# Optimization experiments

Measured on AMD Instinct MI355X. Metric: run time of the kernel, lower is better.

## Reference

```python
import jax, jax.numpy as jnp
import numpy as np

N0, N1 = 30000, 20000
N = N0 + N1
E = 400000
H0, H1, H2 = 4, 4, 1
DH = 64            # num_hidden
NC = 16            # num_classes
IN = 128           # per-type input feature dim
SLOPE = 0.2        # leaky relu negative slope


def setup_inputs() -> dict:
    key = jax.random.key(0)
    ks = iter(jax.random.split(key, 48))
    rn = lambda shape, s=0.05: jax.random.normal(next(ks), shape, jnp.float32) * s
    ri = lambda shape: jax.random.randint(next(ks), shape, 0, N, jnp.int32)
    inp = {
        'features0': rn((N0, IN), 1.0),
        'features1': rn((N1, IN), 1.0),
        'fc_w0': rn((IN, DH)), 'fc_b0': jnp.zeros((DH,), jnp.float32),
        'fc_w1': rn((IN, DH)), 'fc_b1': jnp.zeros((DH,), jnp.float32),
        'mix_w': jnp.zeros((2, 3, 2), jnp.float32),  # (n_types, num_layers+1, n_graphs)
        # GATConv params stacked over the 2 relation graphs
        'W0': rn((2, DH, H0 * DH)), 'al0': rn((2, H0, DH), 0.1), 'ar0': rn((2, H0, DH), 0.1), 'b0': jnp.zeros((2, H0 * DH), jnp.float32),
        'W1': rn((2, H0 * DH, H1 * DH)), 'al1': rn((2, H1, DH), 0.1), 'ar1': rn((2, H1, DH), 0.1), 'b1': jnp.zeros((2, H1 * DH), jnp.float32),
        'W2': rn((2, H1 * DH, H2 * NC)), 'al2': rn((2, H2, NC), 0.1), 'ar2': rn((2, H2, NC), 0.1), 'b2': jnp.zeros((2, H2 * NC), jnp.float32),
        'res2': rn((2, H1 * DH, H2 * NC)),  # res_fc for last layer (in != out*heads)
        'src0': ri((E,)), 'dst0': ri((E,)),
        'src1': ri((E,)), 'dst1': ri((E,)),
    }
    return inp


def gat_conv(h, src, dst, W, al, ar, b, H, D, res_mode, res_w, act):
    # h: (N, in)  ->  (N, H, D)
    feat = (h @ W).reshape(N, H, D)
    el = jnp.sum(feat * al, axis=-1)   # (N, H)
    er = jnp.sum(feat * ar, axis=-1)   # (N, H)
    e = jax.nn.leaky_relu(el[src] + er[dst], SLOPE)  # (E, H)
    # edge softmax over incoming edges of each dst node
    m = jax.ops.segment_max(e, dst, num_segments=N)
    ex = jnp.exp(e - m[dst])
    den = jax.ops.segment_sum(ex, dst, num_segments=N)
    alpha = ex / den[dst]                              # (E, H)
    out = jax.ops.segment_sum(feat[src] * alpha[..., None], dst, num_segments=N)
    if res_mode == 'id':
        out = out + h.reshape(N, H, D)
    elif res_mode == 'fc':
        out = out + (h @ res_w).reshape(N, H, D)
    out = out + b.reshape(1, H, D)
    return jax.nn.elu(out) if act else out


def _forward(features0, features1, fc_w0, fc_b0, fc_w1, fc_b1, mix_w,
             W0, al0, ar0, b0, W1, al1, ar1, b1, W2, al2, ar2, b2, res2,
             src0, dst0, src1, dst1):
    nt = jnp.concatenate([jnp.zeros(N0, jnp.int32), jnp.ones(N1, jnp.int32)])
    w = jax.nn.softmax(mix_w, axis=2)  # (types, layers+1, graphs)
    h = jnp.concatenate([features0 @ fc_w0 + fc_b0, features1 @ fc_w1 + fc_b1], axis=0)
    srcs, dsts = (src0, src1), (dst0, dst1)
    layers = [
        (W0, al0, ar0, b0, H0, DH, None, True),
        (W1, al1, ar1, b1, H1, DH, 'id', True),
    ]
    for l, (W, al, ar, b, H, D, rm, act) in enumerate(layers):
        acc = 0.
        for i in range(2):
            o = gat_conv(h, srcs[i], dsts[i], W[i], al[i], ar[i], b[i], H, D, rm, None, act)
            acc = acc + o.reshape(N, H * D) * w[nt, l, i][:, None]
        h = acc
    logits = 0.
    for i in range(2):
        o = gat_conv(h, srcs[i], dsts[i], W2[i], al2[i], ar2[i], b2[i], H2, NC, 'fc', res2[i], False)
        logits = logits + o.mean(axis=1) * w[nt, 2, i][:, None]
    return logits


def reference(features0, features1, fc_w0, fc_b0, fc_w1, fc_b1, mix_w,
              W0, al0, ar0, b0, W1, al1, ar1, b1, W2, al2, ar2, b2, res2,
              src0, dst0, src1, dst1):
    return _forward(features0, features1, fc_w0, fc_b0, fc_w1, fc_b1, mix_w,
                    W0, al0, ar0, b0, W1, al1, ar1, b1, W2, al2, ar2, b2, res2,
                    src0, dst0, src1, dst1)
```

## Files before the change

### kernel.cpp

```cpp
#include <hip/hip_runtime.h>
#include <hip/hip_bf16.h>

#define NN   50000
#define NN0  30000
#define EE   400000
#define NB_SCAN ((NN + 1023) / 1024)
#define NB_E  ((EE + 255) / 256)
#define NRT   3125
#define NGRP  ((NRT + 3) / 4)
#define NGRP2 1563
#define NT0   1875

typedef unsigned short u16;
typedef unsigned int   u32;

typedef __attribute__((ext_vector_type(8))) __bf16 bf16x8;
typedef __attribute__((ext_vector_type(4))) float  f32x4;
typedef __attribute__((ext_vector_type(2))) float  f32x2;

__device__ __forceinline__ float bf2f(u16 u){ return __uint_as_float(((u32)u)<<16); }
__device__ __forceinline__ float lo16(u32 u){ return __uint_as_float(u<<16); }
__device__ __forceinline__ float hi16(u32 u){ return __uint_as_float(u & 0xffff0000u); }
__device__ __forceinline__ u16 f2bf(float f){
  u32 x = __float_as_uint(f);
  x += 0x7fffu + ((x>>16)&1u);
  return (u16)(x>>16);
}
__device__ __forceinline__ float elu_f(float x){ return x>0.f ? x : __expf(x)-1.f; }
__device__ __forceinline__ float lrelu(float x){ return x>0.f ? x : 0.2f*x; }
__device__ __forceinline__ bf16x8 ld_frag(const u16* p){
  uint4 v = *(const uint4*)p;
  return __builtin_bit_cast(bf16x8, v);
}
__device__ __forceinline__ bf16x8 cvt8(const float* p){
  float4 u = ((const float4*)p)[0];
  float4 v = ((const float4*)p)[1];
  u32 w0 = (u32)f2bf(u.x) | ((u32)f2bf(u.y)<<16);
  u32 w1 = (u32)f2bf(u.z) | ((u32)f2bf(u.w)<<16);
  u32 w2 = (u32)f2bf(v.x) | ((u32)f2bf(v.y)<<16);
  u32 w3 = (u32)f2bf(v.z) | ((u32)f2bf(v.w)<<16);
  uint4 r{w0,w1,w2,w3};
  return __builtin_bit_cast(bf16x8, r);
}
__device__ __forceinline__ u32   ld_u16o (const char* b, u32 o){ return *(const u16*)(b + o); }
__device__ __forceinline__ u32   ld_u32o (const char* b, u32 o){ return *(const u32*)(b + o); }
__device__ __forceinline__ float ld_f32o (const char* b, u32 o){ return *(const float*)(b + o); }
__device__ __forceinline__ float4 ld_f4o (const char* b, u32 o){ return *(const float4*)(b + o); }
__device__ __forceinline__ uint4  ld_u4o (const char* b, u32 o){ return *(const uint4*)(b + o); }
__device__ __forceinline__ void acc8pk(f32x2* p, float& den, float x, uint4 f){
  den += x;
  f32x2 xx = {x, x};
  f32x2 t0 = {lo16(f.x), hi16(f.x)};
  f32x2 t1 = {lo16(f.y), hi16(f.y)};
  f32x2 t2 = {lo16(f.z), hi16(f.z)};
  f32x2 t3 = {lo16(f.w), hi16(f.w)};
  p[0] = __builtin_elementwise_fma(t0, xx, p[0]);
  p[1] = __builtin_elementwise_fma(t1, xx, p[1]);
  p[2] = __builtin_elementwise_fma(t2, xx, p[2]);
  p[3] = __builtin_elementwise_fma(t3, xx, p[3]);
}
__device__ __forceinline__ void acc2x4(f32x2* a, f32x2& d01, f32x2& d23, float4 x, u32 w){
  f32x2 v = {lo16(w), hi16(w)};
  f32x2 x0 = {x.x, x.x}, x1 = {x.y, x.y}, x2 = {x.z, x.z}, x3 = {x.w, x.w};
  a[0] = __builtin_elementwise_fma(v, x0, a[0]);
  a[1] = __builtin_elementwise_fma(v, x1, a[1]);
  a[2] = __builtin_elementwise_fma(v, x2, a[2]);
  a[3] = __builtin_elementwise_fma(v, x3, a[3]);
  f32x2 p01 = {x.x, x.y}, p23 = {x.z, x.w};
  d01 += p01; d23 += p23;
}

__global__ __launch_bounds__(256) void k_prepAll(
    const float* __restrict__ mix_w, float* __restrict__ wsoft,
    const float* __restrict__ W0, u16* __restrict__ W0p,
    const float* __restrict__ W1, u16* __restrict__ W1p,
    const float* __restrict__ W2, const float* __restrict__ res2, u16* __restrict__ W2p,
    const float* __restrict__ fcw0, const float* __restrict__ fcw1, u16* __restrict__ Fp,
    const float* __restrict__ al0, const float* __restrict__ ar0,
    const float* __restrict__ fcb0, const float* __restrict__ fcb1,
    u16* __restrict__ V2p, float* __restrict__ bV,
    int* __restrict__ zeros)
{
  __shared__ float V[64];
  if (blockIdx.x >= 100){
    int b = blockIdx.x - 100;
    int tt = b>>4, cl = b&15;
    int which = cl>>3, g = (cl>>2)&1, h = cl&3;
    int t = threadIdx.x;
    const float* sel = (which ? ar0 : al0) + (size_t)(g*4+h)*64;
    if (t < 64){
      const float* Wrow = W0 + (size_t)g*16384 + (size_t)t*256 + h*64;
      float s = 0.f;
      #pragma unroll 8
      for (int d=0; d<64; d++) s = fmaf(Wrow[d], sel[d], s);
      V[t] = s;
    }
    __syncthreads();
    if (t < 128){
      const float* fw = tt ? fcw1 : fcw0;
      float s = 0.f;
      #pragma unroll 8
      for (int d=0; d<64; d++) s = fmaf(fw[(size_t)t*64 + d], V[d], s);
      int kb = t>>5, q = (t>>3)&3, j = t&7;
      V2p[(size_t)tt*2048 + ((size_t)kb*64 + q*16 + cl)*8 + j] = f2bf(s);
      if (t == 0){
        const float* fbp = tt ? fcb1 : fcb0;
        float sb = 0.f;
        #pragma unroll 8
        for (int d=0; d<64; d++) sb = fmaf(fbp[d], V[d], sb);
        bV[tt*16 + cl] = sb;
      }
    }
    return;
  }
  int t = blockIdx.x*256 + threadIdx.x;
  for (int z = t; z < 4*NN; z += 100*256) zeros[z] = 0;
  if (t < 6){
    float a0 = mix_w[t*2+0], a1 = mix_w[t*2+1];
    float mx = fmaxf(a0,a1);
    float e0 = __expf(a0-mx), e1 = __expf(a1-mx);
    wsoft[t*2+0] = e0/(e0+e1); wsoft[t*2+1] = e1/(e0+e1);
  }
  if (t < 4096){
    int gg = t>>11, fi = t&2047;
    int lane = fi&63, kb = (fi>>6)&1, ct = fi>>7;
    int q = lane>>4, c = lane&15;
    const float* src = W0 + (size_t)gg*16384;
    u16* o = W0p + (size_t)gg*16384 + (size_t)fi*8;
    #pragma unroll
    for (int j=0;j<8;j++) o[j] = f2bf(src[(size_t)(kb*32+q*8+j)*256 + ct*16 + c]);
  } else if (t < 20480){
    int u = t - 4096;
    int gg = u>>13, fi = u&8191;
    int lane = fi&63, kb = (fi>>6)&7, ct = fi>>9;
    int q = lane>>4, c = lane&15;
    const float* src = W1 + (size_t)gg*65536;
    u16* o = W1p + (size_t)gg*65536 + (size_t)fi*8;
    #pragma unroll
    for (int j=0;j<8;j++) o[j] = f2bf(src[(size_t)(kb*32+q*8+j)*256 + ct*16 + c]);
  } else if (t < 22528){
    int fi = t - 20480;
    int lane = fi&63, kb = (fi>>6)&7, ct = fi>>9;
    int q = lane>>4, c = lane&15;
    int cl = ct*16 + c;
    int i = cl>>5, which = (cl>>4)&1;
    const float* src = which ? res2 : W2;
    u16* o = W2p + (size_t)fi*8;
    #pragma unroll
    for (int j=0;j<8;j++) o[j] = f2bf(src[(size_t)i*4096 + (size_t)(kb*32+q*8+j)*16 + (cl&15)]);
  } else if (t < 24576){
    int u = t - 22528;
    int tt = u>>10, fi = u&1023;
    int lane = fi&63, kb = (fi>>6)&3, ct = fi>>8;
    int q = lane>>4, c = lane&15;
    const float* src = tt ? fcw1 : fcw0;
    u16* o = Fp + (size_t)tt*8192 + (size_t)fi*8;
    #pragma unroll
    for (int j=0;j<8;j++) o[j] = f2bf(src[(size_t)(kb*32+q*8+j)*64 + ct*16 + c]);
  }
}

__global__ __launch_bounds__(256) void k_inpcnt(
    const float* __restrict__ f0, const float* __restrict__ f1,
    const u16* __restrict__ Fp, const float* __restrict__ fb0, const float* __restrict__ fb1,
    const u16* __restrict__ V2p, const float* __restrict__ bV,
    u16* __restrict__ h0, float* __restrict__ elA, float* __restrict__ erA,
    const int* __restrict__ d0, const int* __restrict__ d1, int* __restrict__ cnt2)
{
  if (blockIdx.x >= NGRP){
    int u = blockIdx.x - NGRP;
    int g = u / NB_E;
    int t = (u % NB_E)*256 + threadIdx.x;
    if (t < EE) atomicAdd(&cnt2[g*NN + (g ? d1[t] : d0[t])], 1);
    return;
  }
  int wv = threadIdx.x>>6, ln = threadIdx.x&63;
  int ti = blockIdx.x*4 + wv;
  if (ti >= NRT) return;
  int q = ln>>4, c = ln&15;
  int type = (ti < NT0) ? 0 : 1;
  const float* F = type ? f1 : f0;
  int rbase = type ? (ti*16 - NN0) : ti*16;
  const u16* Bg = Fp + (size_t)type*8192;
  const u16* Vg = V2p + (size_t)type*2048;
  const float* bb = type ? fb1 : fb0;
  f32x4 acc[4] = {};
  f32x4 accE = {};
  const float* Ap = F + (size_t)(rbase + c)*128;
  #pragma unroll
  for (int kb=0; kb<4; kb++){
    bf16x8 a = cvt8(Ap + kb*32 + q*8);
    #pragma unroll
    for (int ct=0; ct<4; ct++){
      bf16x8 b = ld_frag(Bg + ((size_t)(ct*4+kb)*64 + ln)*8);
      acc[ct] = __builtin_amdgcn_mfma_f32_16x16x32_bf16(a, b, acc[ct], 0,0,0);
    }
    bf16x8 bv_ = ld_frag(Vg + ((size_t)kb*64 + ln)*8);
    accE = __builtin_amdgcn_mfma_f32_16x16x32_bf16(a, bv_, accE, 0,0,0);
  }
  #pragma unroll
  for (int ct=0; ct<4; ct++){
    float bvs = bb[ct*16+c];
    #pragma unroll
    for (int j=0;j<4;j++){
      int row = ti*16 + q*4 + j;
      h0[(size_t)row*64 + ct*16 + c] = f2bf(acc[ct][j] + bvs);
    }
  }
  int which = c>>3, gg = (c>>2)&1, hh = c&3;
  float bVv = bV[type*16 + c];
  float* dst = (which ? erA : elA) + (size_t)gg*NN*4;
  #pragma unroll
  for (int j=0;j<4;j++){
    int row = ti*16 + q*4 + j;
    dst[row*4 + hh] = accE[j] + bVv;
  }
}

__global__ __launch_bounds__(1024) void k_scan1(const int* __restrict__ cnt2,
                                                int* __restrict__ row2, int* __restrict__ bsum){
  __shared__ int wsum[16];
  int g = blockIdx.y;
  int lane = threadIdx.x & 63, wid = threadIdx.x >> 6;
  int i = blockIdx.x*1024 + threadIdx.x;
  int v = (i < NN) ? cnt2[g*NN + i] : 0;
  int x = v;
  #pragma unroll
  for (int off = 1; off < 64; off <<= 1){
    int y = __shfl_up(x, off, 64);
    if (lane >= off) x += y;
  }
  if (lane == 63) wsum[wid] = x;
  __syncthreads();
  if (wid == 0 && lane < 16){
    int s = wsum[lane];
    #pragma unroll
    for (int off = 1; off < 16; off <<= 1){
      int y = __shfl_up(s, off, 16);
      if (lane >= off) s += y;
    }
    wsum[lane] = s;
  }
  __syncthreads();
  int incl = x + (wid ? wsum[wid-1] : 0);
  if (i < NN) row2[(size_t)g*(NN+1) + i] = incl - v;
  if (threadIdx.x == 1023) bsum[g*NB_SCAN + blockIdx.x] = incl;
}

__global__ __launch_bounds__(1024) void k_scan3(int* __restrict__ row2,
                                                const int* __restrict__ bsum){
  __shared__ int base;
  int g = blockIdx.y;
  if (threadIdx.x < 64){
    int lane = threadIdx.x;
    int v = (lane < (int)blockIdx.x) ? bsum[g*NB_SCAN + lane] : 0;
    #pragma unroll
    for (int off = 32; off; off >>= 1) v += __shfl_xor(v, off, 64);
    if (lane == 0) base = v;
  }
  __syncthreads();
  int i = blockIdx.x*1024 + threadIdx.x;
  if (i < NN) row2[(size_t)g*(NN+1) + i] += base;
  if (blockIdx.x == 0 && threadIdx.x == 0) row2[(size_t)g*(NN+1) + NN] = EE;
}

__global__ void k_scatter2(const int* __restrict__ s0, const int* __restrict__ d0,
                           const int* __restrict__ s1, const int* __restrict__ d1,
                           const int* __restrict__ row2, int* __restrict__ fill2,
                           u16* __restrict__ col2, u16* __restrict__ dstOf){
  int t = blockIdx.x*256 + threadIdx.x;
  int g = blockIdx.y;
  if (t >= EE) return;
  int d = g ? d1[t] : d0[t];
  int s = g ? s1[t] : s0[t];
  int pos = atomicAdd(&fill2[g*NN + d], 1);
  size_t slot = (size_t)g*EE + row2[(size_t)g*(NN+1) + d] + pos;
  col2[slot]  = (u16)s;
  dstOf[slot] = (u16)d;
}

__global__ void k_alpha4(const u16* __restrict__ col2, const u16* __restrict__ dstOf,
                         const float* __restrict__ el, const float* __restrict__ er,
                         size_t elStride, float* __restrict__ xbuf){
  int t = blockIdx.x*256 + threadIdx.x;
  int g = blockIdx.y;
  if (t >= EE) return;
  size_t slot = (size_t)g*EE + t;
  u32 s = col2[slot], d = dstOf[slot];
  const char* elg = (const char*)(el + (size_t)g*elStride);
  const char* erg = (const char*)(er + (size_t)g*elStride);
  float4 e4 = ld_f4o(elg, s<<4);
  float4 r4 = ld_f4o(erg, d<<4);
  float4 x;
  x.x = __expf(lrelu(e4.x + r4.x));
  x.y = __expf(lrelu(e4.y + r4.y));
  x.z = __expf(lrelu(e4.z + r4.z));
  x.w = __expf(lrelu(e4.w + r4.w));
  ((float4*)xbuf)[slot] = x;
}

__global__ __launch_bounds__(128) void k_agg0(
    const int* __restrict__ row2, const u16* __restrict__ col2,
    const float* __restrict__ xbuf, const u16* __restrict__ h0,
    u16* __restrict__ aggB, size_t aggStride)
{
  int wv = threadIdx.x>>6, ln = threadIdx.x&63;
  int n = blockIdx.x*2 + wv;
  int half = ln>>5, l32 = ln&31;
  u32 coloff = (u32)l32<<2;
  const char* cl0 = (const char*)col2;
  const char* cl1 = (const char*)(col2 + EE);
  const char* xb0 = (const char*)xbuf;
  const char* xb1 = xb0 + (size_t)EE*16;
  const char* hp  = (const char*)h0;
  int b0_ = row2[n], e0_ = row2[n+1];
  int b1_ = row2[(NN+1)+n], e1_ = row2[(NN+1)+n+1];
  int n0 = e0_-b0_, n1 = e1_-b1_;
  int mx = n0>n1 ? n0 : n1;
  int iters = (mx+3)>>2;
  f32x2 aA[4] = {}; f32x2 aB[4] = {};
  f32x2 dA01 = {}, dA23 = {}, dB01 = {}, dB23 = {};
  int k0 = b0_+half, k1 = b1_+half;
  for (int it=0; it<iters; ++it){
    int i0=k0, i1=k0+2, j0=k1, j1=k1+2;
    bool v00=i0<e0_, v01=i1<e0_, v10=j0<e1_, v11=j1<e1_;
    u32 ci0=v00?(u32)i0:0u, ci1=v01?(u32)i1:0u, cj0=v10?(u32)j0:0u, cj1=v11?(u32)j1:0u;
    u32 sA0=ld_u16o(cl0,ci0<<1), sA1=ld_u16o(cl0,ci1<<1);
    u32 sB0=ld_u16o(cl1,cj0<<1), sB1=ld_u16o(cl1,cj1<<1);
    float4 z = {0.f,0.f,0.f,0.f};
    float4 xA0 = v00 ? ld_f4o(xb0,ci0<<4) : z;
    float4 xA1 = v01 ? ld_f4o(xb0,ci1<<4) : z;
    float4 xB0 = v10 ? ld_f4o(xb1,cj0<<4) : z;
    float4 xB1 = v11 ? ld_f4o(xb1,cj1<<4) : z;
    u32 wA0 = ld_u32o(hp,(sA0<<7)+coloff);
    u32 wA1 = ld_u32o(hp,(sA1<<7)+coloff);
    u32 wB0 = ld_u32o(hp,(sB0<<7)+coloff);
    u32 wB1 = ld_u32o(hp,(sB1<<7)+coloff);
    acc2x4(aA, dA01, dA23, xA0, wA0);
    acc2x4(aA, dA01, dA23, xA1, wA1);
    acc2x4(aB, dB01, dB23, xB0, wB0);
    acc2x4(aB, dB01, dB23, xB1, wB1);
    k0+=4; k1+=4;
  }
  #pragma unroll
  for (int u=0;u<4;u++){
    aA[u].x += __shfl_xor(aA[u].x,32,64); aA[u].y += __shfl_xor(aA[u].y,32,64);
    aB[u].x += __shfl_xor(aB[u].x,32,64); aB[u].y += __shfl_xor(aB[u].y,32,64);
  }
  dA01.x += __shfl_xor(dA01.x,32,64); dA01.y += __shfl_xor(dA01.y,32,64);
  dA23.x += __shfl_xor(dA23.x,32,64); dA23.y += __shfl_xor(dA23.y,32,64);
  dB01.x += __shfl_xor(dB01.x,32,64); dB01.y += __shfl_xor(dB01.y,32,64);
  dB23.x += __shfl_xor(dB23.x,32,64); dB23.y += __shfl_xor(dB23.y,32,64);
  if (!half){
    bool hg0 = e0_ > b0_, hg1 = e1_ > b1_;
    float iA[4] = { hg0?1.f/dA01.x:0.f, hg0?1.f/dA01.y:0.f, hg0?1.f/dA23.x:0.f, hg0?1.f/dA23.y:0.f };
    float iB[4] = { hg1?1.f/dB01.x:0.f, hg1?1.f/dB01.y:0.f, hg1?1.f/dB23.x:0.f, hg1?1.f/dB23.y:0.f };
    u32* og0 = (u32*)(aggB + (size_t)n*256);
    u32* og1 = (u32*)(aggB + aggStride + (size_t)n*256);
    #pragma unroll
    for (int h=0;h<4;h++){
      u32 w0 = (u32)f2bf(aA[h].x*iA[h]) | ((u32)f2bf(aA[h].y*iA[h])<<16);
      og0[h*32 + l32] = w0;
      u32 w1 = (u32)f2bf(aB[h].x*iB[h]) | ((u32)f2bf(aB[h].y*iB[h])<<16);
      og1[h*32 + l32] = w1;
    }
  }
}

__global__ __launch_bounds__(256) void k_head0(
    const u16* __restrict__ aggB, size_t aggStride,
    const u16* __restrict__ W0p, const float* __restrict__ b0,
    const float* __restrict__ wsoft, u16* __restrict__ h1)
{
  int wv = threadIdx.x>>6, ln = threadIdx.x&63;
  int bg = blockIdx.x;
  int hbase = (bg / NGRP)*2;
  int ti = (bg % NGRP)*4 + wv;
  if (ti >= NRT) return;
  int q = ln>>4, c = ln&15;
  int type = (ti < NT0) ? 0 : 1;
  float wg0 = wsoft[type*6 + 0];
  float wg1 = wsoft[type*6 + 1];
  for (int h=hbase; h<hbase+2; h++){
    f32x4 acc[2][4] = {};
    #pragma unroll
    for (int g=0; g<2; g++){
      const u16* Ap = aggB + (size_t)g*aggStride + (size_t)(ti*16 + c)*256 + h*64 + q*8;
      const u16* Bg = W0p + (size_t)g*16384;
      #pragma unroll
      for (int kb=0; kb<2; kb++){
        bf16x8 a = ld_frag(Ap + kb*32);
        #pragma unroll
        for (int ct=0; ct<4; ct++){
          int ctg = h*4 + ct;
          bf16x8 b = ld_frag(Bg + ((size_t)(ctg*2 + kb)*64 + ln)*8);
          acc[g][ct] = __builtin_amdgcn_mfma_f32_16x16x32_bf16(a, b, acc[g][ct], 0,0,0);
        }
      }
    }
    #pragma unroll
    for (int ct=0; ct<4; ct++){
      int colg = h*64 + ct*16 + c;
      float bb0 = b0[colg], bb1 = b0[256 + colg];
      #pragma unroll
      for (int j=0;j<4;j++){
        int row = ti*16 + q*4 + j;
        float o = wg0*elu_f(acc[0][ct][j] + bb0) + wg1*elu_f(acc[1][ct][j] + bb1);
        h1[(size_t)row*256 + colg] = f2bf(o);
      }
    }
  }
}

template<int K>
__global__ __launch_bounds__(256) void k_gemm4(
    const u16* __restrict__ A,
    const u16* __restrict__ Bp, size_t bpStride,
    const float* __restrict__ al, const float* __restrict__ ar, int alStride,
    u16* __restrict__ feat, size_t featStride,
    float* __restrict__ el, float* __restrict__ er, size_t elStride)
{
  constexpr int KB = K/32;
  int wv = threadIdx.x>>6, ln = threadIdx.x&63;
  int bid = blockIdx.x;
  int g = bid / NGRP2, grp = bid % NGRP2;
  int split = wv, q = ln>>4, c = ln&15;
  const u16* Bpg = Bp + (size_t)g*bpStride;
  const float* alg = al + (size_t)g*alStride;
  const float* arg = ar + (size_t)g*alStride;
  u16* featg = feat + (size_t)g*featStride;
  float* elg = el + (size_t)g*elStride;
  float* erg = er + (size_t)g*elStride;

  f32x4 acc[2][4] = {};
  int  tbase = grp*2;
  bool valid[2];
  const u16* Ap[2];
  #pragma unroll
  for (int rt=0; rt<2; rt++){
    int ti = tbase + rt;
    valid[rt] = (ti < NRT);
    if (!valid[rt]) ti = NRT-1;
    Ap[rt] = A + (size_t)(ti*16 + c)*K + q*8;
  }
  const u16* Bbase = Bpg + ((size_t)(split*4)*KB*64 + ln)*8;

  #pragma unroll 2
  for (int kb=0; kb<KB; kb++){
    bf16x8 b[4], a[2];
    #pragma unroll
    for (int ct=0; ct<4; ct++) b[ct] = ld_frag(Bbase + (size_t)(ct*KB + kb)*64*8);
    #pragma unroll
    for (int rt=0; rt<2; rt++) a[rt] = ld_frag(Ap[rt] + kb*32);
    #pragma unroll
    for (int rt=0; rt<2; rt++)
      #pragma unroll
      for (int ct=0; ct<4; ct++)
        acc[rt][ct] = __builtin_amdgcn_mfma_f32_16x16x32_bf16(a[rt], b[ct], acc[rt][ct], 0,0,0);
  }

  float alv[4], arv[4];
  #pragma unroll
  for (int ct=0;ct<4;ct++){
    int cg = (split*4+ct)*16 + c;
    alv[ct] = alg[cg]; arv[ct] = arg[cg];
  }
  #pragma unroll
  for (int rt=0; rt<2; rt++){
    if (!valid[rt]) continue;
    int row0 = (tbase+rt)*16;
    #pragma unroll
    for (int j=0;j<4;j++){
      float ep=0.f, rp=0.f;
      #pragma unroll
      for (int ct=0;ct<4;ct++){ ep += acc[rt][ct][j]*alv[ct]; rp += acc[rt][ct][j]*arv[ct]; }
      #pragma unroll
      for (int off=8; off; off>>=1){ ep += __shfl_xor(ep,off,16); rp += __shfl_xor(rp,off,16); }
      int row = row0 + q*4 + j;
      if (c==0){ elg[row*4+split]=ep; erg[row*4+split]=rp; }
      #pragma unroll
      for (int ct=0;ct<4;ct++)
        featg[(size_t)row*256 + (split*4+ct)*16 + c] = f2bf(acc[rt][ct][j]);
    }
  }
}

template<int RES>
__global__ __launch_bounds__(128) void k_aggNF(
    const int* __restrict__ row2, const u16* __restrict__ col2,
    const float* __restrict__ xbuf,
    const u16* __restrict__ feat, size_t featStride,
    const u16* __restrict__ hres, const float* __restrict__ bias,
    const float* __restrict__ wsoft, int l,
    u16* __restrict__ hout)
{
  int wv = threadIdx.x>>6, ln = threadIdx.x&63;
  int n = blockIdx.x*2 + wv;
  int half = ln>>5, l32 = ln&31;
  int hh = l32>>3;
  u32 rowoff = (u32)l32<<4;
  u32 hhb    = (u32)hh<<2;
  int type = (n<NN0)?0:1;
  const char* cl0 = (const char*)col2;
  const char* cl1 = (const char*)(col2 + EE);
  const char* x0p = (const char*)xbuf;
  const char* x1p = x0p + (size_t)EE*16;
  const char* fp0 = (const char*)feat;
  const char* fp1 = (const char*)(feat + featStride);
  int b0_ = row2[n], e0_ = row2[n+1];
  int b1_ = row2[(NN+1)+n], e1_ = row2[(NN+1)+n+1];
  int n0 = e0_-b0_, n1 = e1_-b1_;
  int mx = n0>n1 ? n0 : n1;
  int iters = (mx+3)>>2;
  f32x2 pA[4] = {}; f32x2 pB[4] = {};
  float denA = 0.f, denB = 0.f;
  int k0 = b0_+half, k1 = b1_+half;
  for (int it=0; it<iters; ++it){
    int i0=k0, i1=k0+2, j0=k1, j1=k1+2;
    bool v00=i0<e0_, v01=i1<e0_, v10=j0<e1_, v11=j1<e1_;
    u32 ci0=v00?(u32)i0:0u, ci1=v01?(u32)i1:0u, cj0=v10?(u32)j0:0u, cj1=v11?(u32)j1:0u;
    u32 sA0=ld_u16o(cl0,ci0<<1), sA1=ld_u16o(cl0,ci1<<1);
    u32 sB0=ld_u16o(cl1,cj0<<1), sB1=ld_u16o(cl1,cj1<<1);
    float xA0 = v00 ? ld_f32o(x0p,(ci0<<4)+hhb) : 0.f;
    float xA1 = v01 ? ld_f32o(x0p,(ci1<<4)+hhb) : 0.f;
    float xB0 = v10 ? ld_f32o(x1p,(cj0<<4)+hhb) : 0.f;
    float xB1 = v11 ? ld_f32o(x1p,(cj1<<4)+hhb) : 0.f;
    uint4 fA0 = ld_u4o(fp0,(sA0<<9)+rowoff);
    uint4 fA1 = ld_u4o(fp0,(sA1<<9)+rowoff);
    uint4 fB0 = ld_u4o(fp1,(sB0<<9)+rowoff);
    uint4 fB1 = ld_u4o(fp1,(sB1<<9)+rowoff);
    acc8pk(pA, denA, xA0, fA0);
    acc8pk(pA, denA, xA1, fA1);
    acc8pk(pB, denB, xB0, fB0);
    acc8pk(pB, denB, xB1, fB1);
    k0+=4; k1+=4;
  }
  #pragma unroll
  for (int u=0;u<4;u++){
    pA[u].x += __shfl_xor(pA[u].x,32,64); pA[u].y += __shfl_xor(pA[u].y,32,64);
    pB[u].x += __shfl_xor(pB[u].x,32,64); pB[u].y += __shfl_xor(pB[u].y,32,64);
  }
  denA += __shfl_xor(denA,32,64);
  denB += __shfl_xor(denB,32,64);
  if (!half){
    float accA[8], accB[8];
    #pragma unroll
    for (int u=0;u<4;u++){
      accA[2*u]=pA[u].x; accA[2*u+1]=pA[u].y;
      accB[2*u]=pB[u].x; accB[2*u+1]=pB[u].y;
    }
    float inv0 = (e0_>b0_) ? 1.0f/denA : 0.f;
    float inv1 = (e1_>b1_) ? 1.0f/denB : 0.f;
    const float4* bp0 = (const float4*)bias;
    const float4* bp1 = (const float4*)(bias + 256);
    float4 bva = bp0[l32*2], bvb = bp0[l32*2+1];
    float4 bwa = bp1[l32*2], bwb = bp1[l32*2+1];
    float bb0[8] = {bva.x,bva.y,bva.z,bva.w,bvb.x,bvb.y,bvb.z,bvb.w};
    float bb1[8] = {bwa.x,bwa.y,bwa.z,bwa.w,bwb.x,bwb.y,bwb.z,bwb.w};
    float w0 = wsoft[type*6 + l*2 + 0];
    float w1 = wsoft[type*6 + l*2 + 1];
    float r[8] = {0.f,0.f,0.f,0.f,0.f,0.f,0.f,0.f};
    if (RES){
      uint4 rr = ((const uint4*)hres)[(size_t)n*32 + l32];
      r[0]=lo16(rr.x); r[1]=hi16(rr.x); r[2]=lo16(rr.y); r[3]=hi16(rr.y);
      r[4]=lo16(rr.z); r[5]=hi16(rr.z); r[6]=lo16(rr.w); r[7]=hi16(rr.w);
    }
    u16 ov[8];
    #pragma unroll
    for (int j=0;j<8;j++){
      float c = accA[j]*inv0 + bb0[j] + r[j];
      float e = accB[j]*inv1 + bb1[j] + r[j];
      ov[j] = f2bf(w0*elu_f(c) + w1*elu_f(e));
    }
    uint4 o;
    o.x = (u32)ov[0] | ((u32)ov[1]<<16);
    o.y = (u32)ov[2] | ((u32)ov[3]<<16);
    o.z = (u32)ov[4] | ((u32)ov[5]<<16);
    o.w = (u32)ov[6] | ((u32)ov[7]<<16);
    ((uint4*)hout)[(size_t)n*32 + l32] = o;
  }
}

__global__ __launch_bounds__(256) void k_gemm2(
    const u16* __restrict__ A, const u16* __restrict__ Bp,
    const float* __restrict__ al2, const float* __restrict__ ar2,
    u16* __restrict__ feat16, float* __restrict__ resb,
    float* __restrict__ el2, float* __restrict__ er2)
{
  int wv = threadIdx.x>>6, ln = threadIdx.x&63;
  int wt = blockIdx.x*4 + wv;
  if (wt >= NRT) return;
  int row0 = wt*16;
  int q = ln>>4, c = ln&15;
  f32x4 acc[4] = {};
  const u16* Ap = A + (size_t)(row0 + c)*256 + q*8;
  #pragma unroll
  for (int kb=0; kb<8; kb++){
    bf16x8 a = ld_frag(Ap + kb*32);
    #pragma unroll
    for (int t=0;t<4;t++){
      bf16x8 b = ld_frag(Bp + ((size_t)(t*8 + kb)*64 + ln)*8);
      acc[t] = __builtin_amdgcn_mfma_f32_16x16x32_bf16(a, b, acc[t], 0,0,0);
    }
  }
  #pragma unroll
  for (int i=0;i<2;i++){
    float alv = al2[i*16+c], arv = ar2[i*16+c];
    #pragma unroll
    for (int j=0;j<4;j++){
      float ep = acc[2*i][j]*alv, rp = acc[2*i][j]*arv;
      #pragma unroll
      for (int off=8; off; off>>=1){ ep += __shfl_xor(ep,off,16); rp += __shfl_xor(rp,off,16); }
      if (c==0){
        int row = row0 + q*4 + j;
        el2[(size_t)i*NN + row] = ep; er2[(size_t)i*NN + row] = rp;
      }
    }
    #pragma unroll
    for (int j=0;j<4;j++){
      int row = row0 + q*4 + j;
      feat16[(size_t)i*NN*16 + (size_t)row*16 + c] = f2bf(acc[2*i][j]);
      resb  [(size_t)i*NN*16 + (size_t)row*16 + c] = acc[2*i+1][j];
    }
  }
}

__global__ __launch_bounds__(256) void k_agg2D(
    const int* __restrict__ row2, const u16* __restrict__ col2,
    const float* __restrict__ el2, const float* __restrict__ er2,
    const u16* __restrict__ feat16, const float* __restrict__ resb,
    const float* __restrict__ b2, const float* __restrict__ wsoft,
    float* __restrict__ out)
{
  int t = threadIdx.x;
  int nl = t>>4, j = t&15;
  int n = blockIdx.x*16 + nl;
  u32 jb = (u32)j<<1;
  int type = (n<NN0)?0:1;
  float o = 0.f;
  #pragma unroll
  for (int i=0;i<2;i++){
    const int* rw = row2 + (size_t)i*(NN+1);
    const char* cl = (const char*)(col2 + (size_t)i*EE);
    const char* elg = (const char*)(el2 + (size_t)i*NN);
    float ern = er2[(size_t)i*NN + n];
    const char* f = (const char*)(feat16 + (size_t)i*NN*16);
    int beg = rw[n], end = rw[n+1];
    float den = 0.f, acc = 0.f;
    int k = beg;
    for (; k+4<=end; k+=4){
      u32 kb = (u32)k<<1;
      u32 s0=ld_u16o(cl,kb), s1=ld_u16o(cl,kb+2), s2=ld_u16o(cl,kb+4), s3=ld_u16o(cl,kb+6);
      float x0 = __expf(lrelu(ld_f32o(elg,s0<<2) + ern));
      float x1 = __expf(lrelu(ld_f32o(elg,s1<<2) + ern));
      float x2 = __expf(lrelu(ld_f32o(elg,s2<<2) + ern));
      float x3 = __expf(lrelu(ld_f32o(elg,s3<<2) + ern));
      float v0 = bf2f((u16)ld_u16o(f,(s0<<5)+jb));
      float v1 = bf2f((u16)ld_u16o(f,(s1<<5)+jb));
      float v2 = bf2f((u16)ld_u16o(f,(s2<<5)+jb));
      float v3 = bf2f((u16)ld_u16o(f,(s3<<5)+jb));
      den += (x0+x1) + (x2+x3);
      acc += x0*v0 + x1*v1 + x2*v2 + x3*v3;
    }
    for (; k<end; k++){
      u32 s = ld_u16o(cl,(u32)k<<1);
      float x = __expf(lrelu(ld_f32o(elg,s<<2) + ern));
      den += x;
      acc = fmaf(x, bf2f((u16)ld_u16o(f,(s<<5)+jb)), acc);
    }
    float inv = (end>beg) ? 1.0f/den : 0.f;
    float oi = acc*inv + b2[i*16+j] + resb[(size_t)i*NN*16 + (size_t)n*16 + j];
    o += oi * wsoft[type*6 + 4 + i];
  }
  out[(size_t)n*16 + j] = o;
}

extern "C" void kernel_launch(void* const* d_in, const int* in_sizes, int n_in,
                              void* d_out, int out_size, void* d_ws, size_t ws_size,
                              hipStream_t stream)
{
  const float* features0 = (const float*)d_in[0];
  const float* features1 = (const float*)d_in[1];
  const float* fc_w0 = (const float*)d_in[2];
  const float* fc_b0 = (const float*)d_in[3];
  const float* fc_w1 = (const float*)d_in[4];
  const float* fc_b1 = (const float*)d_in[5];
  const float* mix_w = (const float*)d_in[6];
  const float* W0  = (const float*)d_in[7];
  const float* al0 = (const float*)d_in[8];
  const float* ar0 = (const float*)d_in[9];
  const float* b0  = (const float*)d_in[10];
  const float* W1  = (const float*)d_in[11];
  const float* al1 = (const float*)d_in[12];
  const float* ar1 = (const float*)d_in[13];
  const float* b1  = (const float*)d_in[14];
  const float* W2  = (const float*)d_in[15];
  const float* al2 = (const float*)d_in[16];
  const float* ar2 = (const float*)d_in[17];
  const float* b2  = (const float*)d_in[18];
  const float* res2= (const float*)d_in[19];
  const int* src[2] = {(const int*)d_in[20], (const int*)d_in[22]};
  const int* dst[2] = {(const int*)d_in[21], (const int*)d_in[23]};
  (void)in_sizes; (void)n_in; (void)out_size; (void)ws_size;

  char* ws = (char*)d_ws;
  size_t off = 0;
  auto alloc = [&](size_t bytes)->char*{
    char* p = ws + off; off += (bytes + 255) & ~(size_t)255; return p;
  };
  float* wsoft = (float*)alloc(64*4);
  u16*   W0p   = (u16*)  alloc((size_t)2*64*256*2);
  u16*   W1p   = (u16*)  alloc((size_t)2*256*256*2);
  u16*   W2p   = (u16*)  alloc((size_t)256*64*2);
  u16*   Fp    = (u16*)  alloc((size_t)2*128*64*2);
  u16*   V2p   = (u16*)  alloc((size_t)2*128*16*2);
  float* bV    = (float*)alloc((size_t)32*4);
  int*   row2  = (int*)  alloc((size_t)2*(NN+1)*4);
  u16*   col2  = (u16*)  alloc((size_t)2*EE*2);
  u16*   dstOf = (u16*)  alloc((size_t)2*EE*2);
  int*   zeros = (int*)  alloc((size_t)4*NN*4);
  int*   cnt2  = zeros;
  int*   fill2 = zeros + 2*NN;
  int*   bsum  = (int*)alloc((size_t)2*NB_SCAN*4);
  u16*   h0    = (u16*)alloc((size_t)NN*64*2);
  u16*   h1    = (u16*)alloc((size_t)NN*256*2);
  u16*   h2    = (u16*)alloc((size_t)NN*256*2);
  float* elA   = (float*)alloc((size_t)2*NN*4*4);
  float* erA   = (float*)alloc((size_t)2*NN*4*4);
  float* xbuf  = (float*)alloc((size_t)2*EE*4*4);
  size_t featStride = (size_t)NN*256;
  size_t off_D = off;
  u16* regionD = (u16*)alloc(2*featStride*2);
  u16* aggB  = regionD;
  u16* featD = regionD;
  u16*   feat16 = (u16*)(ws + off_D);
  float* resb   = (float*)(ws + off_D + (size_t)2*NN*16*2);
  float* el2    = resb + (size_t)2*NN*16;
  float* er2    = el2  + (size_t)2*NN;

  k_prepAll<<<132,256,0,stream>>>(mix_w, wsoft, W0, W0p, W1, W1p, W2, res2, W2p,
                                  fc_w0, fc_w1, Fp, al0, ar0, fc_b0, fc_b1,
                                  V2p, bV, zeros);

  k_inpcnt<<<NGRP + 2*NB_E,256,0,stream>>>(features0, features1, Fp, fc_b0, fc_b1,
                                           V2p, bV, h0, elA, erA,
                                           dst[0], dst[1], cnt2);

  {
    dim3 gS(NB_SCAN, 2), gEb(NB_E, 2);
    k_scan1  <<<gS,1024,0,stream>>>(cnt2, row2, bsum);
    k_scan3  <<<gS,1024,0,stream>>>(row2, bsum);
    k_scatter2<<<gEb,256,0,stream>>>(src[0], dst[0], src[1], dst[1], row2, fill2, col2, dstOf);
  }

  dim3 gE(NB_E, 2);

  k_alpha4<<<gE,256,0,stream>>>(col2, dstOf, elA, erA, (size_t)NN*4, xbuf);
  k_agg0 <<<NN/2,128,0,stream>>>(row2, col2, xbuf, h0, aggB, featStride);
  k_head0<<<2*NGRP,256,0,stream>>>(aggB, featStride, W0p, b0, wsoft, h1);

  k_gemm4<256><<<2*NGRP2,256,0,stream>>>(h1, W1p, (size_t)256*256, al1, ar1, 256,
                                         featD, featStride, elA, erA, (size_t)NN*4);
  k_alpha4<<<gE,256,0,stream>>>(col2, dstOf, elA, erA, (size_t)NN*4, xbuf);
  k_aggNF<1><<<NN/2,128,0,stream>>>(row2, col2, xbuf, featD, featStride,
                                    h1, b1, wsoft, 1, h2);

  k_gemm2<<<NGRP,256,0,stream>>>(h2, W2p, al2, ar2, feat16, resb, el2, er2);
  k_agg2D<<<NN/16,256,0,stream>>>(row2, col2, el2, er2, feat16, resb, b2, wsoft, (float*)d_out);
}
```

Baseline: 423.3 us.

## Fuse layer-1 edge attention computation into aggregation and unroll edge loop by 8

Removes the separate k_alpha4 pass for layer 1 and computes exp(leaky_relu(el[src]+er[dst])) inside k_aggNF from per-node el/er, skipping the write and read of a per-edge xbuf. The edge loop is also unrolled to four edges per half-wave per graph, which keeps more gathers in flight. The softmax skips the max subtraction, as the prior xbuf path apparently did as well. The cost is extra exp work and more register pressure in the aggregation kernel.

```diff
diff --git a/kernel.cpp b/kernel.cpp
--- a/kernel.cpp
+++ b/kernel.cpp
@@ -27,7 +27,7 @@
   return (u16)(x>>16);
 }
 __device__ __forceinline__ float elu_f(float x){ return x>0.f ? x : __expf(x)-1.f; }
-__device__ __forceinline__ float lrelu(float x){ return x>0.f ? x : 0.2f*x; }
+__device__ __forceinline__ float lrelu(float x){ return fmaxf(x, 0.2f*x); }
 __device__ __forceinline__ bf16x8 ld_frag(const u16* p){
   uint4 v = *(const uint4*)p;
   return __builtin_bit_cast(bf16x8, v);
@@ -488,7 +488,7 @@
 template<int RES>
 __global__ __launch_bounds__(128) void k_aggNF(
     const int* __restrict__ row2, const u16* __restrict__ col2,
-    const float* __restrict__ xbuf,
+    const float* __restrict__ el, const float* __restrict__ er,
     const u16* __restrict__ feat, size_t featStride,
     const u16* __restrict__ hres, const float* __restrict__ bias,
     const float* __restrict__ wsoft, int l,
@@ -503,37 +503,58 @@
   int type = (n<NN0)?0:1;
   const char* cl0 = (const char*)col2;
   const char* cl1 = (const char*)(col2 + EE);
-  const char* x0p = (const char*)xbuf;
-  const char* x1p = x0p + (size_t)EE*16;
+  const char* el0 = (const char*)el;
+  const char* el1 = el0 + (size_t)NN*16;
+  const char* er0 = (const char*)er;
+  const char* er1 = er0 + (size_t)NN*16;
   const char* fp0 = (const char*)feat;
   const char* fp1 = (const char*)(feat + featStride);
   int b0_ = row2[n], e0_ = row2[n+1];
   int b1_ = row2[(NN+1)+n], e1_ = row2[(NN+1)+n+1];
+  float ern0 = ld_f32o(er0,((u32)n<<4)+hhb);
+  float ern1 = ld_f32o(er1,((u32)n<<4)+hhb);
   int n0 = e0_-b0_, n1 = e1_-b1_;
   int mx = n0>n1 ? n0 : n1;
-  int iters = (mx+3)>>2;
+  int iters = (mx+7)>>3;
   f32x2 pA[4] = {}; f32x2 pB[4] = {};
   float denA = 0.f, denB = 0.f;
   int k0 = b0_+half, k1 = b1_+half;
   for (int it=0; it<iters; ++it){
-    int i0=k0, i1=k0+2, j0=k1, j1=k1+2;
-    bool v00=i0<e0_, v01=i1<e0_, v10=j0<e1_, v11=j1<e1_;
-    u32 ci0=v00?(u32)i0:0u, ci1=v01?(u32)i1:0u, cj0=v10?(u32)j0:0u, cj1=v11?(u32)j1:0u;
-    u32 sA0=ld_u16o(cl0,ci0<<1), sA1=ld_u16o(cl0,ci1<<1);
-    u32 sB0=ld_u16o(cl1,cj0<<1), sB1=ld_u16o(cl1,cj1<<1);
-    float xA0 = v00 ? ld_f32o(x0p,(ci0<<4)+hhb) : 0.f;
-    float xA1 = v01 ? ld_f32o(x0p,(ci1<<4)+hhb) : 0.f;
-    float xB0 = v10 ? ld_f32o(x1p,(cj0<<4)+hhb) : 0.f;
-    float xB1 = v11 ? ld_f32o(x1p,(cj1<<4)+hhb) : 0.f;
-    uint4 fA0 = ld_u4o(fp0,(sA0<<9)+rowoff);
-    uint4 fA1 = ld_u4o(fp0,(sA1<<9)+rowoff);
-    uint4 fB0 = ld_u4o(fp1,(sB0<<9)+rowoff);
-    uint4 fB1 = ld_u4o(fp1,(sB1<<9)+rowoff);
+    int i0=k0, i1=k0+2, i2=k0+4, i3=k0+6;
+    int j0=k1, j1=k1+2, j2=k1+4, j3=k1+6;
+    bool vA0=i0<e0_, vA1=i1<e0_, vA2=i2<e0_, vA3=i3<e0_;
+    bool vB0=j0<e1_, vB1=j1<e1_, vB2=j2<e1_, vB3=j3<e1_;
+    u32 cA0=vA0?(u32)i0:0u, cA1=vA1?(u32)i1:0u, cA2=vA2?(u32)i2:0u, cA3=vA3?(u32)i3:0u;
+    u32 cB0=vB0?(u32)j0:0u, cB1=vB1?(u32)j1:0u, cB2=vB2?(u32)j2:0u, cB3=vB3?(u32)j3:0u;
+    u32 sA0=ld_u16o(cl0,cA0<<1), sA1=ld_u16o(cl0,cA1<<1);
+    u32 sA2=ld_u16o(cl0,cA2<<1), sA3=ld_u16o(cl0,cA3<<1);
+    u32 sB0=ld_u16o(cl1,cB0<<1), sB1=ld_u16o(cl1,cB1<<1);
+    u32 sB2=ld_u16o(cl1,cB2<<1), sB3=ld_u16o(cl1,cB3<<1);
+    float eA0=ld_f32o(el0,(sA0<<4)+hhb), eA1=ld_f32o(el0,(sA1<<4)+hhb);
+    float eA2=ld_f32o(el0,(sA2<<4)+hhb), eA3=ld_f32o(el0,(sA3<<4)+hhb);
+    float eB0=ld_f32o(el1,(sB0<<4)+hhb), eB1=ld_f32o(el1,(sB1<<4)+hhb);
+    float eB2=ld_f32o(el1,(sB2<<4)+hhb), eB3=ld_f32o(el1,(sB3<<4)+hhb);
+    uint4 fA0=ld_u4o(fp0,(sA0<<9)+rowoff), fA1=ld_u4o(fp0,(sA1<<9)+rowoff);
+    uint4 fA2=ld_u4o(fp0,(sA2<<9)+rowoff), fA3=ld_u4o(fp0,(sA3<<9)+rowoff);
+    uint4 fB0=ld_u4o(fp1,(sB0<<9)+rowoff), fB1=ld_u4o(fp1,(sB1<<9)+rowoff);
+    uint4 fB2=ld_u4o(fp1,(sB2<<9)+rowoff), fB3=ld_u4o(fp1,(sB3<<9)+rowoff);
+    float xA0 = vA0 ? __expf(lrelu(eA0+ern0)) : 0.f;
+    float xA1 = vA1 ? __expf(lrelu(eA1+ern0)) : 0.f;
+    float xA2 = vA2 ? __expf(lrelu(eA2+ern0)) : 0.f;
+    float xA3 = vA3 ? __expf(lrelu(eA3+ern0)) : 0.f;
+    float xB0 = vB0 ? __expf(lrelu(eB0+ern1)) : 0.f;
+    float xB1 = vB1 ? __expf(lrelu(eB1+ern1)) : 0.f;
+    float xB2 = vB2 ? __expf(lrelu(eB2+ern1)) : 0.f;
+    float xB3 = vB3 ? __expf(lrelu(eB3+ern1)) : 0.f;
     acc8pk(pA, denA, xA0, fA0);
     acc8pk(pA, denA, xA1, fA1);
+    acc8pk(pA, denA, xA2, fA2);
+    acc8pk(pA, denA, xA3, fA3);
     acc8pk(pB, denB, xB0, fB0);
     acc8pk(pB, denB, xB1, fB1);
-    k0+=4; k1+=4;
+    acc8pk(pB, denB, xB2, fB2);
+    acc8pk(pB, denB, xB3, fB3);
+    k0+=8; k1+=8;
   }
   #pragma unroll
   for (int u=0;u<4;u++){
@@ -761,8 +782,7 @@
 
   k_gemm4<256><<<2*NGRP2,256,0,stream>>>(h1, W1p, (size_t)256*256, al1, ar1, 256,
                                          featD, featStride, elA, erA, (size_t)NN*4);
-  k_alpha4<<<gE,256,0,stream>>>(col2, dstOf, elA, erA, (size_t)NN*4, xbuf);
-  k_aggNF<1><<<NN/2,128,0,stream>>>(row2, col2, xbuf, featD, featStride,
+  k_aggNF<1><<<NN/2,128,0,stream>>>(row2, col2, elA, erA, featD, featStride,
                                     h1, b1, wsoft, 1, h2);
 
   k_gemm2<<<NGRP,256,0,stream>>>(h2, W2p, al2, ar2, feat16, resb, el2, er2);
```

After: 421.8 us. No clear change (-0.4%).
